# Optimization experiments

Hardware: AMD Instinct MI355X
Metric: run time of the kernel (lower is better)

Reference implementation:

```python
import jax, jax.numpy as jnp
import numpy as np

W_RNN = 768
DEC_H = 256
TAGS = 2
TAG_EM = 32


def setup_inputs() -> dict:
    key = jax.random.key(0)
    ks = jax.random.split(key, 8)
    B, T = 64, 512
    in_size = W_RNN + TAG_EM  # 800
    aff_in = W_RNN + DEC_H    # 1024
    sents_vec = jax.random.normal(ks[0], (B, T, W_RNN), dtype=jnp.float32)
    mask_cls = jnp.ones((B, T), dtype=jnp.float32)
    # xavier-uniform-ish init for weights, zeros for biases (matches param_init)
    def xavier(k, shape):
        fan_in, fan_out = shape[1], shape[0]
        lim = float(np.sqrt(6.0 / (fan_in + fan_out)))
        return jax.random.uniform(k, shape, jnp.float32, -lim, lim)
    Wih = xavier(ks[1], (4 * DEC_H, in_size))
    Whh = xavier(ks[2], (4 * DEC_H, DEC_H))
    bih = jnp.zeros((4 * DEC_H,), jnp.float32)
    bhh = jnp.zeros((4 * DEC_H,), jnp.float32)
    Waff = xavier(ks[3], (TAGS, aff_in))
    baff = jnp.zeros((TAGS,), jnp.float32)
    tag_em = xavier(ks[4], (TAGS, TAG_EM))
    return {"sents_vec": sents_vec, "mask_cls": mask_cls, "Wih": Wih,
            "Whh": Whh, "bih": bih, "bhh": bhh, "Waff": Waff,
            "baff": baff, "tag_em": tag_em}


def reference(sents_vec, mask_cls, Wih, Whh, bih, bhh, Waff, baff, tag_em):
    # Dropout is treated in eval mode (identity), as is standard for a
    # deterministic correctness baseline.
    B, T, D = sents_vec.shape
    H = DEC_H
    h0 = jnp.zeros((B, H), sents_vec.dtype)
    go = jnp.zeros((B, TAG_EM), sents_vec.dtype)

    Hs = jnp.swapaxes(sents_vec, 0, 1)        # [T, B, D]
    Ms = jnp.swapaxes(mask_cls, 0, 1)[..., None]  # [T, B, 1]

    def step(carry, xs):
        h, c, yem = carry
        Hi, mi = xs
        x = jnp.concatenate([yem, Hi], axis=1)            # [B, 800]
        gates = x @ Wih.T + h @ Whh.T + (bih + bhh)       # [B, 4H]
        i_g, f_g, g_g, o_g = jnp.split(gates, 4, axis=1)  # torch LSTMCell order
        c_new = jax.nn.sigmoid(f_g) * c + jax.nn.sigmoid(i_g) * jnp.tanh(g_g)
        h_new = jax.nn.sigmoid(o_g) * jnp.tanh(c_new)
        score = jnp.concatenate([h_new, Hi], axis=1) @ Waff.T + baff  # [B, TAGS]
        pred = jnp.argmax(score, axis=-1)                 # [B]
        yem_new = tag_em[pred]                            # [B, TAG_EM]
        h_out = h_new * mi + h * (1.0 - mi)
        c_out = c_new * mi + c * (1.0 - mi)
        return (h_out, c_out, yem_new), score

    _, scores = jax.lax.scan(step, (h0, h0, go), (Hs, Ms))  # [T, B, TAGS]
    scores = jnp.swapaxes(scores, 0, 1)                      # [B, T, TAGS]
    return jax.nn.log_softmax(scores, axis=2)
```

## Files before the change

### kernel.cpp

```cpp
#include <hip/hip_runtime.h>
#include <cstdint>
#include <cstddef>

#define TT 512
#define BB 64
#define HH 256
#define NG 1024
#define DI 768
#define KY 32

#define LDP 56

typedef __attribute__((ext_vector_type(8))) short bfrag_t;
typedef __attribute__((ext_vector_type(4))) float f4_t;

__device__ __forceinline__ float sigf(float x) {
    return __fdividef(1.f, 1.f + __expf(-x));
}
__device__ __forceinline__ float tanhfast(float x) {
    return fmaf(2.f, sigf(2.f * x), -1.f);
}
__device__ __forceinline__ unsigned short bf_hi(float x) {
    return (unsigned short)(__float_as_uint(x) >> 16);
}
__device__ __forceinline__ float bf_hi_f(float x) {
    return __uint_as_float(__float_as_uint(x) & 0xffff0000u);
}

__global__ __launch_bounds__(256) void kgemm2(
    const float* __restrict__ sents, const float* __restrict__ Wih,
    const float* __restrict__ bih, const float* __restrict__ bhh,
    float* __restrict__ gpre, int t0)
{
    __shared__ unsigned short Ah[128 * LDP], Al[128 * LDP];
    __shared__ unsigned short Bh[128 * LDP], Bl[128 * LDP];

    const int tid = threadIdx.x;
    const int nb = blockIdx.x;
    const int mb = blockIdx.y;
    const int wv = tid >> 6, lane = tid & 63;
    const int wm = (wv >> 1) * 64, wn = (wv & 1) * 64;
    const int fl = lane & 15, quad = lane >> 4;

    f4_t acc[4][4];
#pragma unroll
    for (int mi = 0; mi < 4; ++mi)
#pragma unroll
        for (int ni = 0; ni < 4; ++ni) acc[mi][ni] = (f4_t)0.f;

    const int sr = tid >> 1, sk = (tid & 1) * 16;
    const int gr = mb * 128 + sr;
    const float* aptr = sents + ((size_t)(gr & 63) * TT + t0 + (gr >> 6)) * DI + sk;
    const float* bptr = Wih + (size_t)(nb * 128 + sr) * 800 + KY + sk;

    for (int k0 = 0; k0 < DI; k0 += 32) {
        float4 av[4], bv[4];
#pragma unroll
        for (int i = 0; i < 4; ++i) {
            av[i] = *(const float4*)(aptr + k0 + i * 4);
            bv[i] = *(const float4*)(bptr + k0 + i * 4);
        }
        __syncthreads();
#pragma unroll
        for (int i = 0; i < 4; ++i) {
            ushort4 h4, l4;
            h4.x = bf_hi(av[i].x); l4.x = bf_hi(av[i].x - bf_hi_f(av[i].x));
            h4.y = bf_hi(av[i].y); l4.y = bf_hi(av[i].y - bf_hi_f(av[i].y));
            h4.z = bf_hi(av[i].z); l4.z = bf_hi(av[i].z - bf_hi_f(av[i].z));
            h4.w = bf_hi(av[i].w); l4.w = bf_hi(av[i].w - bf_hi_f(av[i].w));
            *(ushort4*)&Ah[sr * LDP + sk + i * 4] = h4;
            *(ushort4*)&Al[sr * LDP + sk + i * 4] = l4;
            h4.x = bf_hi(bv[i].x); l4.x = bf_hi(bv[i].x - bf_hi_f(bv[i].x));
            h4.y = bf_hi(bv[i].y); l4.y = bf_hi(bv[i].y - bf_hi_f(bv[i].y));
            h4.z = bf_hi(bv[i].z); l4.z = bf_hi(bv[i].z - bf_hi_f(bv[i].z));
            h4.w = bf_hi(bv[i].w); l4.w = bf_hi(bv[i].w - bf_hi_f(bv[i].w));
            *(ushort4*)&Bh[sr * LDP + sk + i * 4] = h4;
            *(ushort4*)&Bl[sr * LDP + sk + i * 4] = l4;
        }
        __syncthreads();

        bfrag_t ah[4], al2[4], bh[4], bl2[4];
#pragma unroll
        for (int mi = 0; mi < 4; ++mi) {
            int row = wm + mi * 16 + fl;
            ah[mi]  = *(const bfrag_t*)&Ah[row * LDP + quad * 8];
            al2[mi] = *(const bfrag_t*)&Al[row * LDP + quad * 8];
        }
#pragma unroll
        for (int ni = 0; ni < 4; ++ni) {
            int col = wn + ni * 16 + fl;
            bh[ni]  = *(const bfrag_t*)&Bh[col * LDP + quad * 8];
            bl2[ni] = *(const bfrag_t*)&Bl[col * LDP + quad * 8];
        }
#pragma unroll
        for (int mi = 0; mi < 4; ++mi)
#pragma unroll
            for (int ni = 0; ni < 4; ++ni) {
                acc[mi][ni] = __builtin_amdgcn_mfma_f32_16x16x32_bf16(
                    ah[mi], bh[ni], acc[mi][ni], 0, 0, 0);
                acc[mi][ni] = __builtin_amdgcn_mfma_f32_16x16x32_bf16(
                    ah[mi], bl2[ni], acc[mi][ni], 0, 0, 0);
                acc[mi][ni] = __builtin_amdgcn_mfma_f32_16x16x32_bf16(
                    al2[mi], bh[ni], acc[mi][ni], 0, 0, 0);
            }
    }

#pragma unroll
    for (int ni = 0; ni < 4; ++ni) {
        int gcol = nb * 128 + wn + ni * 16 + fl;
        float bias = bih[gcol] + bhh[gcol];
#pragma unroll
        for (int mi = 0; mi < 4; ++mi) {
            int grow = mb * 128 + wm + mi * 16 + quad * 4;
#pragma unroll
            for (int r = 0; r < 4; ++r)
                gpre[(size_t)(grow + r) * NG + gcol] = acc[mi][ni][r] + bias;
        }
    }
}

__global__ __launch_bounds__(256) void kshi(
    const float* __restrict__ sents, const float* __restrict__ Waff,
    const float* __restrict__ baff, float* __restrict__ shi, int t0)
{
    const int tid = threadIdx.x;
    const int lane = tid & 63;
    const int r = blockIdx.x * 4 + (tid >> 6);
    const int b = r & 63, tl = r >> 6;
    const float* hi = sents + ((size_t)b * TT + t0 + tl) * DI;
    float p0 = 0.f, p1 = 0.f;
#pragma unroll
    for (int kk = 0; kk < 12; ++kk) {
        int k = kk * 64 + lane;
        float x = hi[k];
        p0 = fmaf(x, Waff[HH + k], p0);
        p1 = fmaf(x, Waff[NG + HH + k], p1);
    }
#pragma unroll
    for (int off = 32; off >= 1; off >>= 1) {
        p0 += __shfl_xor(p0, off, 64);
        p1 += __shfl_xor(p1, off, 64);
    }
    if (lane == 0) {
        shi[(size_t)r * 2 + 0] = p0 + baff[0];
        shi[(size_t)r * 2 + 1] = p1 + baff[1];
    }
}

__global__ void kinit(unsigned long long* __restrict__ hbox) {
    hbox[(size_t)blockIdx.x * 512 + threadIdx.x] = 0ull;
}

__global__ __launch_bounds__(512, 1) void krec3(
    const float* __restrict__ gpre,
    const float* __restrict__ shi,
    const float* __restrict__ Whh,
    const float* __restrict__ mask,
    float* __restrict__ out,
    float* __restrict__ sh, float* __restrict__ sc, int* __restrict__ sp,
    unsigned long long* __restrict__ hbox,
    const float* __restrict__ Wih, const float* __restrict__ tag,
    const float* __restrict__ Waff,
    int t0, int Tc, int first)
{
    const int blk = blockIdx.x;
    const int g = blk >> 6, b = blk & 63;
    const int tid = threadIdx.x;
    const int w = tid >> 6, lane = tid & 63;
    const int jl = lane & 7, kq = lane >> 3;
    const int jh = w * 8 + jl;
    const int jglob = g * 64 + jh;

    __shared__ float hk[8 * 36];
    __shared__ float hnS[HH];
    __shared__ float P[2][4][64];
    __shared__ float tg[2][KY];
    __shared__ float red[8][2];

    float4 wreg[4][8];
#pragma unroll
    for (int gt = 0; gt < 4; ++gt) {
        const float4* src = (const float4*)(Whh + (size_t)(gt * HH + jglob) * HH + kq * 32);
#pragma unroll
        for (int kk = 0; kk < 8; ++kk) wreg[gt][kk] = src[kk];
    }

    const int sdim = w * 32 + (lane & 31);
    const int stag = lane >> 5;
    const float waffR = Waff[(size_t)stag * NG + sdim];

    if (tid < 2 * KY) tg[tid >> 5][tid & 31] = tag[tid];
    __syncthreads();
    {
        int r = tid >> 8, rem = tid & 255, gt = rem >> 6, j2 = rem & 63;
        int row = gt * HH + g * 64 + j2;
        const float4* wr = (const float4*)(Wih + (size_t)row * 800);
        float s = 0.f;
#pragma unroll
        for (int kk = 0; kk < 8; ++kk) {
            float4 v = wr[kk];
            s = fmaf(v.x, tg[r][kk * 4 + 0], s);
            s = fmaf(v.y, tg[r][kk * 4 + 1], s);
            s = fmaf(v.z, tg[r][kk * 4 + 2], s);
            s = fmaf(v.w, tg[r][kk * 4 + 3], s);
        }
        P[r][gt][j2] = s;
    }

    float creg; int pred;
    if (first) {
        creg = 0.f; pred = -1;
        if (tid < 72) ((float4*)hk)[tid] = make_float4(0.f, 0.f, 0.f, 0.f);
    } else {
        creg = sc[(size_t)b * HH + jglob];
        pred = sp[b];
        if (tid < HH) hk[(tid >> 5) * 36 + (tid & 31)] = sh[(size_t)b * HH + tid];
    }
    __syncthreads();

    float cgp0, cgp1, cgp2, cgp3, cmi, cs0, cs1;
    {
        const float* gp = gpre + ((size_t)0 * BB + b) * NG;
        cgp0 = gp[0 * HH + jglob]; cgp1 = gp[1 * HH + jglob];
        cgp2 = gp[2 * HH + jglob]; cgp3 = gp[3 * HH + jglob];
        cmi = mask[(size_t)b * TT + t0];
        const float* s2 = shi + ((size_t)0 * BB + b) * 2;
        cs0 = s2[0]; cs1 = s2[1];
    }

    for (int tl = 0; tl < Tc; ++tl) {
        const int t = t0 + tl;
        const int p = t & 1;

        float pv0 = 0.f, pv1 = 0.f, pv2 = 0.f, pv3 = 0.f;
        if (pred >= 0) {
            pv0 = P[pred][0][jh]; pv1 = P[pred][1][jh];
            pv2 = P[pred][2][jh]; pv3 = P[pred][3][jh];
        }

        float a0 = 0.f, a1 = 0.f, a2 = 0.f, a3 = 0.f;
        const float4* h4 = (const float4*)(hk + kq * 36);
#pragma unroll
        for (int kk = 0; kk < 8; ++kk) {
            float4 hv = h4[kk];
            a0 = fmaf(wreg[0][kk].x, hv.x, a0); a0 = fmaf(wreg[0][kk].y, hv.y, a0);
            a0 = fmaf(wreg[0][kk].z, hv.z, a0); a0 = fmaf(wreg[0][kk].w, hv.w, a0);
            a1 = fmaf(wreg[1][kk].x, hv.x, a1); a1 = fmaf(wreg[1][kk].y, hv.y, a1);
            a1 = fmaf(wreg[1][kk].z, hv.z, a1); a1 = fmaf(wreg[1][kk].w, hv.w, a1);
            a2 = fmaf(wreg[2][kk].x, hv.x, a2); a2 = fmaf(wreg[2][kk].y, hv.y, a2);
            a2 = fmaf(wreg[2][kk].z, hv.z, a2); a2 = fmaf(wreg[2][kk].w, hv.w, a2);
            a3 = fmaf(wreg[3][kk].x, hv.x, a3); a3 = fmaf(wreg[3][kk].y, hv.y, a3);
            a3 = fmaf(wreg[3][kk].z, hv.z, a3); a3 = fmaf(wreg[3][kk].w, hv.w, a3);
        }
        a0 += __shfl_xor(a0, 8, 64); a0 += __shfl_xor(a0, 16, 64); a0 += __shfl_xor(a0, 32, 64);
        a1 += __shfl_xor(a1, 8, 64); a1 += __shfl_xor(a1, 16, 64); a1 += __shfl_xor(a1, 32, 64);
        a2 += __shfl_xor(a2, 8, 64); a2 += __shfl_xor(a2, 16, 64); a2 += __shfl_xor(a2, 32, 64);
        a3 += __shfl_xor(a3, 8, 64); a3 += __shfl_xor(a3, 16, 64); a3 += __shfl_xor(a3, 32, 64);

        float gi = a0 + cgp0 + pv0;
        float gf = a1 + cgp1 + pv1;
        float gg = a2 + cgp2 + pv2;
        float go = a3 + cgp3 + pv3;
        float ig = sigf(gi), fg = sigf(gf);
        float g2 = tanhfast(gg), og = sigf(go);
        float cn = fmaf(fg, creg, ig * g2);
        float hn = og * tanhfast(cn);
        float mi = cmi;
        float s2v0 = cs0, s2v1 = cs1;
        creg = cn * mi + creg * (1.f - mi);

        if (kq == 0) {
            unsigned long long wd =
                ((unsigned long long)__float_as_uint(hn) << 32) | (unsigned)(t + 1);
            __hip_atomic_store(&hbox[((size_t)(p * BB + b) * 4 + g) * 64 + jh], wd,
                               __ATOMIC_RELAXED, __HIP_MEMORY_SCOPE_AGENT);
            hnS[jglob] = hn;
        }

        if (tl + 1 < Tc) {
            const float* gp2 = gpre + ((size_t)(tl + 1) * BB + b) * NG;
            cgp0 = gp2[0 * HH + jglob]; cgp1 = gp2[1 * HH + jglob];
            cgp2 = gp2[2 * HH + jglob]; cgp3 = gp2[3 * HH + jglob];
            cmi = mask[(size_t)b * TT + t + 1];
            const float* s2n = shi + ((size_t)(tl + 1) * BB + b) * 2;
            cs0 = s2n[0]; cs1 = s2n[1];
        }

        if (tid < 192) {
            int pg = (g + 1 + (tid >> 6)) & 3, j2 = tid & 63;
            const unsigned long long* wp = &hbox[((size_t)(p * BB + b) * 4 + pg) * 64 + j2];
            unsigned long long wv;
            do {
                wv = __hip_atomic_load(wp, __ATOMIC_RELAXED, __HIP_MEMORY_SCOPE_AGENT);
            } while ((unsigned)wv != (unsigned)(t + 1));
            hnS[pg * 64 + j2] = __uint_as_float((unsigned)(wv >> 32));
        }
        __syncthreads();

        if (tid < HH) {
            int idx = (tid >> 5) * 36 + (tid & 31);
            float hold = hk[idx];
            hk[idx] = hnS[tid] * mi + hold * (1.f - mi);
        }
        float prod = hnS[sdim] * waffR;
        prod += __shfl_xor(prod, 1, 64);
        prod += __shfl_xor(prod, 2, 64);
        prod += __shfl_xor(prod, 4, 64);
        prod += __shfl_xor(prod, 8, 64);
        prod += __shfl_xor(prod, 16, 64);
        if ((lane & 31) == 0) red[w][stag] = prod;
        __syncthreads();

        float s0 = red[0][0];
        s0 += red[1][0]; s0 += red[2][0]; s0 += red[3][0];
        s0 += red[4][0]; s0 += red[5][0]; s0 += red[6][0]; s0 += red[7][0];
        float s1 = red[0][1];
        s1 += red[1][1]; s1 += red[2][1]; s1 += red[3][1];
        s1 += red[4][1]; s1 += red[5][1]; s1 += red[6][1]; s1 += red[7][1];
        float ts0 = s0 + s2v0, ts1 = s1 + s2v1;
        pred = (ts1 > ts0) ? 1 : 0;
        if (g == 0 && tid == 0) {
            float m = fmaxf(ts0, ts1);
            float lse = m + log1pf(expf(-fabsf(ts0 - ts1)));
            float* op = out + ((size_t)b * TT + t) * 2;
            op[0] = ts0 - lse; op[1] = ts1 - lse;
        }
    }

    if (kq == 0) {
        sh[(size_t)b * HH + jglob] = hk[(jglob >> 5) * 36 + (jglob & 31)];
        sc[(size_t)b * HH + jglob] = creg;
    }
    if (g == 0 && tid == 0) sp[b] = pred;
}

extern "C" void kernel_launch(void* const* d_in, const int* in_sizes, int n_in,
                              void* d_out, int out_size, void* d_ws, size_t ws_size,
                              hipStream_t stream) {
    (void)in_sizes; (void)n_in; (void)out_size;
    const float* sents = (const float*)d_in[0];
    const float* mask  = (const float*)d_in[1];
    const float* Wih   = (const float*)d_in[2];
    const float* Whh   = (const float*)d_in[3];
    const float* bih   = (const float*)d_in[4];
    const float* bhh   = (const float*)d_in[5];
    const float* Waff  = (const float*)d_in[6];
    const float* baff  = (const float*)d_in[7];
    const float* tag   = (const float*)d_in[8];
    float* out = (float*)d_out;

    const size_t fixed = (size_t)BB * HH * 4 * 2
                       + BB * 4
                       + (size_t)2 * BB * 4 * 64 * 8
                       + 4096;
    int Tc = 8;
    const int cands[7] = {512, 256, 128, 64, 32, 16, 8};
    for (int i = 0; i < 7; ++i) {
        size_t need = (size_t)cands[i] * BB * NG * 4
                    + (size_t)cands[i] * BB * 2 * 4
                    + fixed;
        if (need <= ws_size) { Tc = cands[i]; break; }
    }

    char* wsp = (char*)d_ws;
    float* gpre = (float*)wsp; wsp += (size_t)Tc * BB * NG * 4;
    float* shiw = (float*)wsp; wsp += (size_t)Tc * BB * 2 * 4;
    float* shst = (float*)wsp; wsp += (size_t)BB * HH * 4;
    float* scst = (float*)wsp; wsp += (size_t)BB * HH * 4;
    int*   spst = (int*)wsp;   wsp += BB * 4;
    unsigned long long* hbox = (unsigned long long*)wsp;

    kinit<<<dim3(64), 512, 0, stream>>>(hbox);

    const int nch = TT / Tc;
    for (int c = 0; c < nch; ++c) {
        const int t0 = c * Tc;
        kgemm2<<<dim3(8, Tc * 64 / 128), 256, 0, stream>>>(sents, Wih, bih, bhh, gpre, t0);
        kshi<<<dim3(Tc * 16), 256, 0, stream>>>(sents, Waff, baff, shiw, t0);
        krec3<<<dim3(256), 512, 0, stream>>>(gpre, shiw, Whh, mask, out,
                                             shst, scst, spst, hbox,
                                             Wih, tag, Waff, t0, Tc, (c == 0) ? 1 : 0);
    }
}
```

Measured before the change: 1.436 ms.

## Pre-split Wih to bf16 hi/lo and restructure recurrence step synchronization

Adds a one-time kernel that splits the input-projection weights into bf16 high/low halves, so the GEMM loads pre-converted B tiles instead of converting fp32 weights on every tile load. The recurrent kernel now keeps the hidden-state slice in registers, double-buffers the new-h shared array, and replaces the second block barrier with per-wave flag-tagged atomic slots for the score reduction. That reduction is deferred and overlapped with the next step's Whh matvec. Together these are meant to shorten the serial per-timestep critical path, at the cost of extra workspace, spin-waits on shared memory, and more complex epilogue handling.

```diff
diff --git a/kernel.cpp b/kernel.cpp
--- a/kernel.cpp
+++ b/kernel.cpp
@@ -27,13 +27,25 @@
     return __uint_as_float(__float_as_uint(x) & 0xffff0000u);
 }
 
+__global__ __launch_bounds__(256) void kconvW(
+    const float* __restrict__ Wih,
+    unsigned short* __restrict__ WH, unsigned short* __restrict__ WL)
+{
+    const int col = blockIdx.x * 256 + threadIdx.x;
+    const int row = blockIdx.y;
+    float v = Wih[(size_t)row * 800 + KY + col];
+    WH[(size_t)row * DI + col] = bf_hi(v);
+    WL[(size_t)row * DI + col] = bf_hi(v - bf_hi_f(v));
+}
+
 __global__ __launch_bounds__(256) void kgemm2(
-    const float* __restrict__ sents, const float* __restrict__ Wih,
+    const float* __restrict__ sents,
+    const unsigned short* __restrict__ WH, const unsigned short* __restrict__ WL,
     const float* __restrict__ bih, const float* __restrict__ bhh,
     float* __restrict__ gpre, int t0)
 {
-    __shared__ unsigned short Ah[128 * LDP], Al[128 * LDP];
-    __shared__ unsigned short Bh[128 * LDP], Bl[128 * LDP];
+    __shared__ __align__(16) unsigned short Ah[128 * LDP], Al[128 * LDP];
+    __shared__ __align__(16) unsigned short Bh[128 * LDP], Bl[128 * LDP];
 
     const int tid = threadIdx.x;
     const int nb = blockIdx.x;
@@ -51,15 +63,17 @@
     const int sr = tid >> 1, sk = (tid & 1) * 16;
     const int gr = mb * 128 + sr;
     const float* aptr = sents + ((size_t)(gr & 63) * TT + t0 + (gr >> 6)) * DI + sk;
-    const float* bptr = Wih + (size_t)(nb * 128 + sr) * 800 + KY + sk;
+    const unsigned short* bhp = WH + (size_t)(nb * 128 + sr) * DI + sk;
+    const unsigned short* blp = WL + (size_t)(nb * 128 + sr) * DI + sk;
 
     for (int k0 = 0; k0 < DI; k0 += 32) {
-        float4 av[4], bv[4];
-#pragma unroll
-        for (int i = 0; i < 4; ++i) {
-            av[i] = *(const float4*)(aptr + k0 + i * 4);
-            bv[i] = *(const float4*)(bptr + k0 + i * 4);
-        }
+        float4 av[4];
+#pragma unroll
+        for (int i = 0; i < 4; ++i) av[i] = *(const float4*)(aptr + k0 + i * 4);
+        uint4 bh0 = *(const uint4*)(bhp + k0);
+        uint4 bh1 = *(const uint4*)(bhp + k0 + 8);
+        uint4 bl0 = *(const uint4*)(blp + k0);
+        uint4 bl1 = *(const uint4*)(blp + k0 + 8);
         __syncthreads();
 #pragma unroll
         for (int i = 0; i < 4; ++i) {
@@ -70,13 +84,11 @@
             h4.w = bf_hi(av[i].w); l4.w = bf_hi(av[i].w - bf_hi_f(av[i].w));
             *(ushort4*)&Ah[sr * LDP + sk + i * 4] = h4;
             *(ushort4*)&Al[sr * LDP + sk + i * 4] = l4;
-            h4.x = bf_hi(bv[i].x); l4.x = bf_hi(bv[i].x - bf_hi_f(bv[i].x));
-            h4.y = bf_hi(bv[i].y); l4.y = bf_hi(bv[i].y - bf_hi_f(bv[i].y));
-            h4.z = bf_hi(bv[i].z); l4.z = bf_hi(bv[i].z - bf_hi_f(bv[i].z));
-            h4.w = bf_hi(bv[i].w); l4.w = bf_hi(bv[i].w - bf_hi_f(bv[i].w));
-            *(ushort4*)&Bh[sr * LDP + sk + i * 4] = h4;
-            *(ushort4*)&Bl[sr * LDP + sk + i * 4] = l4;
-        }
+        }
+        *(uint4*)&Bh[sr * LDP + sk + 0] = bh0;
+        *(uint4*)&Bh[sr * LDP + sk + 8] = bh1;
+        *(uint4*)&Bl[sr * LDP + sk + 0] = bl0;
+        *(uint4*)&Bl[sr * LDP + sk + 8] = bl1;
         __syncthreads();
 
         bfrag_t ah[4], al2[4], bh[4], bl2[4];
@@ -151,7 +163,7 @@
     hbox[(size_t)blockIdx.x * 512 + threadIdx.x] = 0ull;
 }
 
-__global__ __launch_bounds__(512, 1) void krec3(
+__global__ __launch_bounds__(512, 1) void krec6(
     const float* __restrict__ gpre,
     const float* __restrict__ shi,
     const float* __restrict__ Whh,
@@ -171,11 +183,10 @@
     const int jh = w * 8 + jl;
     const int jglob = g * 64 + jh;
 
-    __shared__ float hk[8 * 36];
-    __shared__ float hnS[HH];
+    __shared__ float hnS[2][HH];
+    __shared__ unsigned long long redL[8][2];
     __shared__ float P[2][4][64];
     __shared__ float tg[2][KY];
-    __shared__ float red[8][2];
 
     float4 wreg[4][8];
 #pragma unroll
@@ -190,6 +201,7 @@
     const float waffR = Waff[(size_t)stag * NG + sdim];
 
     if (tid < 2 * KY) tg[tid >> 5][tid & 31] = tag[tid];
+    if (tid < 16) ((unsigned long long*)redL)[tid] = 0ull;
     __syncthreads();
     {
         int r = tid >> 8, rem = tid & 255, gt = rem >> 6, j2 = rem & 63;
@@ -208,41 +220,64 @@
     }
 
     float creg; int pred;
+    float4 hoct[8];
     if (first) {
         creg = 0.f; pred = -1;
-        if (tid < 72) ((float4*)hk)[tid] = make_float4(0.f, 0.f, 0.f, 0.f);
+#pragma unroll
+        for (int i = 0; i < 8; ++i) hoct[i] = make_float4(0.f, 0.f, 0.f, 0.f);
     } else {
         creg = sc[(size_t)b * HH + jglob];
         pred = sp[b];
-        if (tid < HH) hk[(tid >> 5) * 36 + (tid & 31)] = sh[(size_t)b * HH + tid];
+        const float4* hs = (const float4*)(sh + (size_t)b * HH + kq * 32);
+#pragma unroll
+        for (int i = 0; i < 8; ++i) hoct[i] = hs[i];
     }
     __syncthreads();
 
     float cgp0, cgp1, cgp2, cgp3, cmi, cs0, cs1;
+    float pmi = 0.f, psv0 = 0.f, psv1 = 0.f;
     {
-        const float* gp = gpre + ((size_t)0 * BB + b) * NG;
+        const float* gp = gpre + (size_t)b * NG;
         cgp0 = gp[0 * HH + jglob]; cgp1 = gp[1 * HH + jglob];
         cgp2 = gp[2 * HH + jglob]; cgp3 = gp[3 * HH + jglob];
         cmi = mask[(size_t)b * TT + t0];
-        const float* s2 = shi + ((size_t)0 * BB + b) * 2;
+        const float* s2 = shi + (size_t)b * 2;
         cs0 = s2[0]; cs1 = s2[1];
     }
 
     for (int tl = 0; tl < Tc; ++tl) {
         const int t = t0 + tl;
         const int p = t & 1;
-
-        float pv0 = 0.f, pv1 = 0.f, pv2 = 0.f, pv3 = 0.f;
-        if (pred >= 0) {
-            pv0 = P[pred][0][jh]; pv1 = P[pred][1][jh];
-            pv2 = P[pred][2][jh]; pv3 = P[pred][3][jh];
+        const unsigned cnt = (unsigned)(t + 1);
+
+        if (tl > 0) {
+            const float4* hp = (const float4*)(&hnS[p ^ 1][kq * 32]);
+#pragma unroll
+            for (int i = 0; i < 8; ++i) {
+                float4 hv = hp[i];
+                hoct[i].x = hv.x * pmi + hoct[i].x * (1.f - pmi);
+                hoct[i].y = hv.y * pmi + hoct[i].y * (1.f - pmi);
+                hoct[i].z = hv.z * pmi + hoct[i].z * (1.f - pmi);
+                hoct[i].w = hv.w * pmi + hoct[i].w * (1.f - pmi);
+            }
+            float pr = hnS[p ^ 1][sdim] * waffR;
+            pr += __shfl_xor(pr, 1, 64);
+            pr += __shfl_xor(pr, 2, 64);
+            pr += __shfl_xor(pr, 4, 64);
+            pr += __shfl_xor(pr, 8, 64);
+            pr += __shfl_xor(pr, 16, 64);
+            if ((lane & 31) == 0) {
+                unsigned long long wd =
+                    ((unsigned long long)__float_as_uint(pr) << 32) | cnt;
+                __hip_atomic_store(&redL[w][stag], wd,
+                                   __ATOMIC_RELAXED, __HIP_MEMORY_SCOPE_WORKGROUP);
+            }
         }
 
         float a0 = 0.f, a1 = 0.f, a2 = 0.f, a3 = 0.f;
-        const float4* h4 = (const float4*)(hk + kq * 36);
 #pragma unroll
         for (int kk = 0; kk < 8; ++kk) {
-            float4 hv = h4[kk];
+            float4 hv = hoct[kk];
             a0 = fmaf(wreg[0][kk].x, hv.x, a0); a0 = fmaf(wreg[0][kk].y, hv.y, a0);
             a0 = fmaf(wreg[0][kk].z, hv.z, a0); a0 = fmaf(wreg[0][kk].w, hv.w, a0);
             a1 = fmaf(wreg[1][kk].x, hv.x, a1); a1 = fmaf(wreg[1][kk].y, hv.y, a1);
@@ -257,6 +292,37 @@
         a2 += __shfl_xor(a2, 8, 64); a2 += __shfl_xor(a2, 16, 64); a2 += __shfl_xor(a2, 32, 64);
         a3 += __shfl_xor(a3, 8, 64); a3 += __shfl_xor(a3, 16, 64); a3 += __shfl_xor(a3, 32, 64);
 
+        if (tl > 0) {
+            float s0 = 0.f, s1 = 0.f;
+#pragma unroll
+            for (int wv = 0; wv < 8; ++wv) {
+                unsigned long long v0, v1;
+                do {
+                    v0 = __hip_atomic_load(&redL[wv][0],
+                                           __ATOMIC_RELAXED, __HIP_MEMORY_SCOPE_WORKGROUP);
+                } while ((unsigned)v0 != cnt);
+                do {
+                    v1 = __hip_atomic_load(&redL[wv][1],
+                                           __ATOMIC_RELAXED, __HIP_MEMORY_SCOPE_WORKGROUP);
+                } while ((unsigned)v1 != cnt);
+                s0 += __uint_as_float((unsigned)(v0 >> 32));
+                s1 += __uint_as_float((unsigned)(v1 >> 32));
+            }
+            float ts0 = s0 + psv0, ts1 = s1 + psv1;
+            pred = (ts1 > ts0) ? 1 : 0;
+            if (g == 0 && tid == 0) {
+                float m = fmaxf(ts0, ts1);
+                float lse = m + log1pf(expf(-fabsf(ts0 - ts1)));
+                float* op = out + ((size_t)b * TT + (t - 1)) * 2;
+                op[0] = ts0 - lse; op[1] = ts1 - lse;
+            }
+        }
+
+        float pv0 = 0.f, pv1 = 0.f, pv2 = 0.f, pv3 = 0.f;
+        if (pred >= 0) {
+            pv0 = P[pred][0][jh]; pv1 = P[pred][1][jh];
+            pv2 = P[pred][2][jh]; pv3 = P[pred][3][jh];
+        }
         float gi = a0 + cgp0 + pv0;
         float gf = a1 + cgp1 + pv1;
         float gg = a2 + cgp2 + pv2;
@@ -265,72 +331,98 @@
         float g2 = tanhfast(gg), og = sigf(go);
         float cn = fmaf(fg, creg, ig * g2);
         float hn = og * tanhfast(cn);
-        float mi = cmi;
-        float s2v0 = cs0, s2v1 = cs1;
-        creg = cn * mi + creg * (1.f - mi);
+        creg = cn * cmi + creg * (1.f - cmi);
 
         if (kq == 0) {
             unsigned long long wd =
-                ((unsigned long long)__float_as_uint(hn) << 32) | (unsigned)(t + 1);
+                ((unsigned long long)__float_as_uint(hn) << 32) | cnt;
             __hip_atomic_store(&hbox[((size_t)(p * BB + b) * 4 + g) * 64 + jh], wd,
                                __ATOMIC_RELAXED, __HIP_MEMORY_SCOPE_AGENT);
-            hnS[jglob] = hn;
-        }
-
+            hnS[p][jglob] = hn;
+        }
+
+        float ngp0 = 0.f, ngp1 = 0.f, ngp2 = 0.f, ngp3 = 0.f;
+        float nmi = 0.f, ns0 = 0.f, ns1 = 0.f;
         if (tl + 1 < Tc) {
             const float* gp2 = gpre + ((size_t)(tl + 1) * BB + b) * NG;
-            cgp0 = gp2[0 * HH + jglob]; cgp1 = gp2[1 * HH + jglob];
-            cgp2 = gp2[2 * HH + jglob]; cgp3 = gp2[3 * HH + jglob];
-            cmi = mask[(size_t)b * TT + t + 1];
+            ngp0 = gp2[0 * HH + jglob]; ngp1 = gp2[1 * HH + jglob];
+            ngp2 = gp2[2 * HH + jglob]; ngp3 = gp2[3 * HH + jglob];
+            nmi = mask[(size_t)b * TT + t + 1];
             const float* s2n = shi + ((size_t)(tl + 1) * BB + b) * 2;
-            cs0 = s2n[0]; cs1 = s2n[1];
+            ns0 = s2n[0]; ns1 = s2n[1];
         }
 
         if (tid < 192) {
             int pg = (g + 1 + (tid >> 6)) & 3, j2 = tid & 63;
-            const unsigned long long* wp = &hbox[((size_t)(p * BB + b) * 4 + pg) * 64 + j2];
+            const unsigned long long* wp =
+                &hbox[((size_t)(p * BB + b) * 4 + pg) * 64 + j2];
             unsigned long long wv;
             do {
                 wv = __hip_atomic_load(wp, __ATOMIC_RELAXED, __HIP_MEMORY_SCOPE_AGENT);
-            } while ((unsigned)wv != (unsigned)(t + 1));
-            hnS[pg * 64 + j2] = __uint_as_float((unsigned)(wv >> 32));
+            } while ((unsigned)wv != cnt);
+            hnS[p][pg * 64 + j2] = __uint_as_float((unsigned)(wv >> 32));
         }
         __syncthreads();
 
-        if (tid < HH) {
-            int idx = (tid >> 5) * 36 + (tid & 31);
-            float hold = hk[idx];
-            hk[idx] = hnS[tid] * mi + hold * (1.f - mi);
-        }
-        float prod = hnS[sdim] * waffR;
-        prod += __shfl_xor(prod, 1, 64);
-        prod += __shfl_xor(prod, 2, 64);
-        prod += __shfl_xor(prod, 4, 64);
-        prod += __shfl_xor(prod, 8, 64);
-        prod += __shfl_xor(prod, 16, 64);
-        if ((lane & 31) == 0) red[w][stag] = prod;
-        __syncthreads();
-
-        float s0 = red[0][0];
-        s0 += red[1][0]; s0 += red[2][0]; s0 += red[3][0];
-        s0 += red[4][0]; s0 += red[5][0]; s0 += red[6][0]; s0 += red[7][0];
-        float s1 = red[0][1];
-        s1 += red[1][1]; s1 += red[2][1]; s1 += red[3][1];
-        s1 += red[4][1]; s1 += red[5][1]; s1 += red[6][1]; s1 += red[7][1];
-        float ts0 = s0 + s2v0, ts1 = s1 + s2v1;
+        pmi = cmi; psv0 = cs0; psv1 = cs1;
+        cgp0 = ngp0; cgp1 = ngp1; cgp2 = ngp2; cgp3 = ngp3;
+        cmi = nmi; cs0 = ns0; cs1 = ns1;
+    }
+
+    {
+        const int pl = (t0 + Tc - 1) & 1;
+        const unsigned fcnt = (unsigned)(t0 + Tc + 1);
+        const float4* hp = (const float4*)(&hnS[pl][kq * 32]);
+#pragma unroll
+        for (int i = 0; i < 8; ++i) {
+            float4 hv = hp[i];
+            hoct[i].x = hv.x * pmi + hoct[i].x * (1.f - pmi);
+            hoct[i].y = hv.y * pmi + hoct[i].y * (1.f - pmi);
+            hoct[i].z = hv.z * pmi + hoct[i].z * (1.f - pmi);
+            hoct[i].w = hv.w * pmi + hoct[i].w * (1.f - pmi);
+        }
+        float pr = hnS[pl][sdim] * waffR;
+        pr += __shfl_xor(pr, 1, 64);
+        pr += __shfl_xor(pr, 2, 64);
+        pr += __shfl_xor(pr, 4, 64);
+        pr += __shfl_xor(pr, 8, 64);
+        pr += __shfl_xor(pr, 16, 64);
+        if ((lane & 31) == 0) {
+            unsigned long long wd =
+                ((unsigned long long)__float_as_uint(pr) << 32) | fcnt;
+            __hip_atomic_store(&redL[w][stag], wd,
+                               __ATOMIC_RELAXED, __HIP_MEMORY_SCOPE_WORKGROUP);
+        }
+        float s0 = 0.f, s1 = 0.f;
+#pragma unroll
+        for (int wv = 0; wv < 8; ++wv) {
+            unsigned long long v0, v1;
+            do {
+                v0 = __hip_atomic_load(&redL[wv][0],
+                                       __ATOMIC_RELAXED, __HIP_MEMORY_SCOPE_WORKGROUP);
+            } while ((unsigned)v0 != fcnt);
+            do {
+                v1 = __hip_atomic_load(&redL[wv][1],
+                                       __ATOMIC_RELAXED, __HIP_MEMORY_SCOPE_WORKGROUP);
+            } while ((unsigned)v1 != fcnt);
+            s0 += __uint_as_float((unsigned)(v0 >> 32));
+            s1 += __uint_as_float((unsigned)(v1 >> 32));
+        }
+        float ts0 = s0 + psv0, ts1 = s1 + psv1;
         pred = (ts1 > ts0) ? 1 : 0;
         if (g == 0 && tid == 0) {
             float m = fmaxf(ts0, ts1);
             float lse = m + log1pf(expf(-fabsf(ts0 - ts1)));
-            float* op = out + ((size_t)b * TT + t) * 2;
+            float* op = out + ((size_t)b * TT + (t0 + Tc - 1)) * 2;
             op[0] = ts0 - lse; op[1] = ts1 - lse;
         }
     }
-
-    if (kq == 0) {
-        sh[(size_t)b * HH + jglob] = hk[(jglob >> 5) * 36 + (jglob & 31)];
-        sc[(size_t)b * HH + jglob] = creg;
-    }
+    if (w == 0 && jl == 0) {
+        float4* dst = (float4*)(sh + (size_t)b * HH + kq * 32);
+#pragma unroll
+        for (int i = 0; i < 8; ++i) dst[i] = hoct[i];
+    }
+    if (kq == 0) sc[(size_t)b * HH + jglob] = creg;
     if (g == 0 && tid == 0) sp[b] = pred;
 }
 
@@ -349,7 +441,9 @@
     const float* tag   = (const float*)d_in[8];
     float* out = (float*)d_out;
 
-    const size_t fixed = (size_t)BB * HH * 4 * 2
+    const size_t wsplit = (size_t)NG * DI * 2 * 2;
+    const size_t fixed = wsplit
+                       + (size_t)BB * HH * 4 * 2
                        + BB * 4
                        + (size_t)2 * BB * 4 * 64 * 8
                        + 4096;
@@ -363,6 +457,8 @@
     }
 
     char* wsp = (char*)d_ws;
+    unsigned short* WH = (unsigned short*)wsp; wsp += (size_t)NG * DI * 2;
+    unsigned short* WL = (unsigned short*)wsp; wsp += (size_t)NG * DI * 2;
     float* gpre = (float*)wsp; wsp += (size_t)Tc * BB * NG * 4;
     float* shiw = (float*)wsp; wsp += (size_t)Tc * BB * 2 * 4;
     float* shst = (float*)wsp; wsp += (size_t)BB * HH * 4;
@@ -370,14 +466,15 @@
     int*   spst = (int*)wsp;   wsp += BB * 4;
     unsigned long long* hbox = (unsigned long long*)wsp;
 
+    kconvW<<<dim3(3, 1024), 256, 0, stream>>>(Wih, WH, WL);
     kinit<<<dim3(64), 512, 0, stream>>>(hbox);
 
     const int nch = TT / Tc;
     for (int c = 0; c < nch; ++c) {
         const int t0 = c * Tc;
-        kgemm2<<<dim3(8, Tc * 64 / 128), 256, 0, stream>>>(sents, Wih, bih, bhh, gpre, t0);
+        kgemm2<<<dim3(8, Tc * 64 / 128), 256, 0, stream>>>(sents, WH, WL, bih, bhh, gpre, t0);
         kshi<<<dim3(Tc * 16), 256, 0, stream>>>(sents, Waff, baff, shiw, t0);
-        krec3<<<dim3(256), 512, 0, stream>>>(gpre, shiw, Whh, mask, out,
+        krec6<<<dim3(256), 512, 0, stream>>>(gpre, shiw, Whh, mask, out,
                                              shst, scst, spst, hbox,
                                              Wih, tag, Waff, t0, Tc, (c == 0) ? 1 : 0);
     }
```

After: 1.709 ms. 19.0% more time.
